# Kernel optimization log

Measured on AMD Instinct MI355X. Metric: run time of the kernel, lower is better.

The kernel has to match this reference:

```python
import jax, jax.numpy as jnp
import numpy as np

V, D, H, L, T_BLOCK = 32000, 1024, 16, 4, 1024
HD = D // H
FF = 4 * D
EPS = 1e-5


def layer_norm(x, w, b):
    mu = jnp.mean(x, axis=-1, keepdims=True)
    var = jnp.mean(jnp.square(x - mu), axis=-1, keepdims=True)
    return (x - mu) * jax.lax.rsqrt(var + EPS) * w + b


def setup_inputs() -> dict:
    key = jax.random.key(0)
    ks = iter(jax.random.split(key, 32))
    s = 0.02
    inp = {
        "idx": jax.random.randint(next(ks), (4, 1024), 0, V, dtype=jnp.int32),
        "tok_emb": jax.random.normal(next(ks), (V, D), jnp.float32) * s,
        "pos_emb": jax.random.normal(next(ks), (T_BLOCK, D), jnp.float32) * s,
        "ln1_w": jnp.ones((L, D), jnp.float32),
        "ln1_b": jnp.zeros((L, D), jnp.float32),
        "wq": jax.random.normal(next(ks), (L, D, D), jnp.float32) * s,
        "wk": jax.random.normal(next(ks), (L, D, D), jnp.float32) * s,
        "wv": jax.random.normal(next(ks), (L, D, D), jnp.float32) * s,
        "wproj": jax.random.normal(next(ks), (L, D, D), jnp.float32) * s,
        "bproj": jnp.zeros((L, D), jnp.float32),
        "ln2_w": jnp.ones((L, D), jnp.float32),
        "ln2_b": jnp.zeros((L, D), jnp.float32),
        "w1": jax.random.normal(next(ks), (L, D, FF), jnp.float32) * s,
        "b1": jnp.zeros((L, FF), jnp.float32),
        "w2": jax.random.normal(next(ks), (L, FF, D), jnp.float32) * s,
        "b2": jnp.zeros((L, D), jnp.float32),
        "lnf_w": jnp.ones((D,), jnp.float32),
        "lnf_b": jnp.zeros((D,), jnp.float32),
        "wout": jax.random.normal(next(ks), (D, V), jnp.float32) * s,
        "bout": jnp.zeros((V,), jnp.float32),
    }
    return inp


def reference(idx, tok_emb, pos_emb, ln1_w, ln1_b, wq, wk, wv, wproj, bproj,
              ln2_w, ln2_b, w1, b1, w2, b2, lnf_w, lnf_b, wout, bout):
    B, T = idx.shape
    x = tok_emb[idx] + pos_emb[:T]  # (B,T,D)
    causal = jnp.tril(jnp.ones((T, T), bool))
    scale = 1.0 / jnp.sqrt(jnp.asarray(HD, x.dtype))
    for l in range(L):
        h = layer_norm(x, ln1_w[l], ln1_b[l])
        q = (h @ wq[l]).reshape(B, T, H, HD)
        k = (h @ wk[l]).reshape(B, T, H, HD)
        v = (h @ wv[l]).reshape(B, T, H, HD)
        scores = jnp.einsum('bqhd,bkhd->bhqk', q, k) * scale
        scores = jnp.where(causal, scores, -jnp.inf)
        weights = jax.nn.softmax(scores, axis=-1)
        attn = jnp.einsum('bhqk,bkhd->bqhd', weights, v).reshape(B, T, D)
        x = x + attn @ wproj[l] + bproj[l]
        h2 = layer_norm(x, ln2_w[l], ln2_b[l])
        x = x + jax.nn.relu(h2 @ w1[l] + b1[l]) @ w2[l] + b2[l]
    x = layer_norm(x, lnf_w, lnf_b)
    logits = x @ wout + bout  # (B,T,V)
    return logits
```

## Files before the change

kernel.cpp:

```cpp
#include <hip/hip_runtime.h>
#include <hip/hip_bf16.h>

#define V_  32000
#define D_  1024
#define H_  16
#define L_  4
#define T_  1024
#define B_  4
#define HD_ 64
#define FF_ 4096
#define M_  4096
#define QP_ 3072

typedef unsigned short u16;
typedef float  f32x4   __attribute__((ext_vector_type(4)));
typedef float  f32x16  __attribute__((ext_vector_type(16)));
typedef __bf16 bf16x8  __attribute__((ext_vector_type(8)));
typedef u16    us8     __attribute__((ext_vector_type(8)));

typedef __attribute__((address_space(1))) void gvoid;
typedef __attribute__((address_space(3))) void lvoid;

__device__ __forceinline__ void glds16(const void* g, void* l) {
  __builtin_amdgcn_global_load_lds((gvoid*)g, (lvoid*)l, 16, 0, 0);
}
__device__ __forceinline__ u16 f2bf(float f) {
  __hip_bfloat16 h = __float2bfloat16(f);
  return reinterpret_cast<u16&>(h);
}

#define BAR() __builtin_amdgcn_s_barrier()
#define VMC(n) asm volatile("s_waitcnt vmcnt(" #n ")" ::: "memory")
#define LGKMC(n) do { asm volatile("s_waitcnt lgkmcnt(" #n ")" ::: "memory"); \
                      __builtin_amdgcn_sched_barrier(0); } while (0)

__global__ __launch_bounds__(256) void embed_kernel(
    const int* __restrict__ idx, const float* __restrict__ tok,
    const float* __restrict__ pos, float* __restrict__ x)
{
  int bt = blockIdx.x;
  int t  = bt & (T_ - 1);
  int id = idx[bt];
  float4 a = ((const float4*)(tok + (size_t)id * D_))[threadIdx.x];
  float4 p = ((const float4*)(pos + (size_t)t  * D_))[threadIdx.x];
  a.x += p.x; a.y += p.y; a.z += p.z; a.w += p.w;
  ((float4*)(x + (size_t)bt * D_))[threadIdx.x] = a;
}

__global__ __launch_bounds__(256) void ln_kernel(
    const float* __restrict__ x, const float* __restrict__ w,
    const float* __restrict__ b, u16* __restrict__ out)
{
  int row = blockIdx.x;
  float4 v = ((const float4*)(x + (size_t)row * D_))[threadIdx.x];
  float s  = v.x + v.y + v.z + v.w;
  float s2 = v.x * v.x + v.y * v.y + v.z * v.z + v.w * v.w;
#pragma unroll
  for (int m = 1; m < 64; m <<= 1) { s += __shfl_xor(s, m); s2 += __shfl_xor(s2, m); }
  __shared__ float ssum[4], ssum2[4];
  int wv = threadIdx.x >> 6;
  if ((threadIdx.x & 63) == 0) { ssum[wv] = s; ssum2[wv] = s2; }
  __syncthreads();
  s  = ssum[0]  + ssum[1]  + ssum[2]  + ssum[3];
  s2 = ssum2[0] + ssum2[1] + ssum2[2] + ssum2[3];
  float mu  = s * (1.f / D_);
  float var = s2 * (1.f / D_) - mu * mu;
  float rs  = rsqrtf(var + 1e-5f);
  float4 wv4 = ((const float4*)w)[threadIdx.x];
  float4 bv4 = ((const float4*)b)[threadIdx.x];
  u16* o = out + (size_t)row * D_ + threadIdx.x * 4;
  o[0] = f2bf((v.x - mu) * rs * wv4.x + bv4.x);
  o[1] = f2bf((v.y - mu) * rs * wv4.y + bv4.y);
  o[2] = f2bf((v.z - mu) * rs * wv4.z + bv4.z);
  o[3] = f2bf((v.w - mu) * rs * wv4.w + bv4.w);
}

__global__ __launch_bounds__(256) void transpose_convert(
    const float* __restrict__ in, u16* __restrict__ out, int R, int C,
    size_t inStride, size_t outStride)
{
  __shared__ float tile[32][33];
  in  += (size_t)blockIdx.z * inStride;
  out += (size_t)blockIdx.z * outStride;
  int c  = blockIdx.x * 32 + threadIdx.x;
  int r0 = blockIdx.y * 32;
#pragma unroll
  for (int j = 0; j < 4; j++)
    tile[threadIdx.y + 8 * j][threadIdx.x] =
        in[(size_t)(r0 + threadIdx.y + 8 * j) * C + c];
  __syncthreads();
  int rr = r0 + threadIdx.x;
  int cb = blockIdx.x * 32;
#pragma unroll
  for (int j = 0; j < 4; j++)
    out[(size_t)(cb + threadIdx.y + 8 * j) * R + rr] =
        f2bf(tile[threadIdx.x][threadIdx.y + 8 * j]);
}

__global__ __launch_bounds__(256) void vtrans_kernel(
    const u16* __restrict__ qkv, u16* __restrict__ vtb)
{
  __shared__ u16 tile[64][72];
  int tt = blockIdx.x, bh = blockIdx.y;
  int b = bh >> 4, h = bh & 15;
  const u16* src = qkv + ((size_t)(b * T_ + tt * 64)) * QP_ + 2 * D_ + h * HD_;
#pragma unroll
  for (int it = 0; it < 2; it++) {
    int u = it * 256 + threadIdx.x;
    int r = u >> 3, c = (u & 7) << 3;
    *(us8*)&tile[r][c] = *(const us8*)&src[(size_t)r * QP_ + c];
  }
  __syncthreads();
#pragma unroll
  for (int it = 0; it < 2; it++) {
    int u = it * 256 + threadIdx.x;
    int d = u >> 3, t8 = (u & 7) << 3;
    us8 v;
#pragma unroll
    for (int j = 0; j < 8; j++) v[j] = tile[t8 + j][d];
    *(us8*)&vtb[((size_t)bh * HD_ + d) * T_ + tt * 64 + t8] = v;
  }
}

template<int EPI>
__global__ __launch_bounds__(256) void gemm_bt(
    const u16* __restrict__ A, const u16* __restrict__ Bt,
    const float* __restrict__ bias, const float* __restrict__ resid,
    void* __restrict__ Cout, int M, int N, int K)
{
  __shared__ u16 As[128 * 32];
  __shared__ u16 Bs[128 * 32];
  const int tid = threadIdx.x;
  const int m0 = blockIdx.x * 128;
  const int n0 = blockIdx.y * 128;
  const int w = tid >> 6, lane = tid & 63, lg = lane >> 4, lr = lane & 15;
  const int wr = w >> 1, wc = w & 1;
  f32x4 acc[4][4] = {};
  const int srow = tid >> 2;
  const int scol = (tid & 3) << 3;
  const u16* ap = A  + (size_t)(m0 + srow) * K + scol;
  const u16* bp = Bt + (size_t)(n0 + srow) * K + scol;
  u16* alds  = &As[tid * 8];
  u16* alds2 = &As[2048 + tid * 8];
  u16* blds  = &Bs[tid * 8];
  u16* blds2 = &Bs[2048 + tid * 8];
  for (int k0 = 0; k0 < K; k0 += 32) {
    __syncthreads();
    glds16(ap + k0,                  alds);
    glds16(ap + (size_t)64 * K + k0, alds2);
    glds16(bp + k0,                  blds);
    glds16(bp + (size_t)64 * K + k0, blds2);
    __syncthreads();
    bf16x8 af[4], bfr[4];
#pragma unroll
    for (int i = 0; i < 4; i++)
      af[i] = *(const bf16x8*)&As[(wr * 64 + i * 16 + lr) * 32 + lg * 8];
#pragma unroll
    for (int j = 0; j < 4; j++)
      bfr[j] = *(const bf16x8*)&Bs[(wc * 64 + j * 16 + lr) * 32 + lg * 8];
#pragma unroll
    for (int i = 0; i < 4; i++)
#pragma unroll
      for (int j = 0; j < 4; j++)
        acc[i][j] = __builtin_amdgcn_mfma_f32_16x16x32_bf16(af[i], bfr[j], acc[i][j], 0, 0, 0);
  }
#pragma unroll
  for (int i = 0; i < 4; i++) {
#pragma unroll
    for (int j = 0; j < 4; j++) {
      int col = n0 + wc * 64 + j * 16 + lr;
      float bv = bias ? bias[col] : 0.f;
#pragma unroll
      for (int r = 0; r < 4; r++) {
        int row = m0 + wr * 64 + i * 16 + lg * 4 + r;
        float val = acc[i][j][r] + bv;
        size_t o = (size_t)row * N + col;
        if (EPI == 0)      ((u16*)Cout)[o]   = f2bf(val);
        else if (EPI == 1) ((u16*)Cout)[o]   = f2bf(val > 0.f ? val : 0.f);
        else if (EPI == 2) ((float*)Cout)[o] = resid[o] + val;
        else               ((float*)Cout)[o] = val;
      }
    }
  }
}

#define CLUSTER(AF, BV, MS) do { \
  __builtin_amdgcn_s_setprio(1); \
  _Pragma("unroll") for (int mq_ = 0; mq_ < 2; ++mq_) \
  _Pragma("unroll") for (int nq_ = 0; nq_ < 2; ++nq_) \
  _Pragma("unroll") for (int kq_ = 0; kq_ < 2; ++kq_) \
    acc[(MS)+mq_][nq_] = __builtin_amdgcn_mfma_f32_32x32x16_bf16( \
        AF[mq_][kq_], BV[nq_][kq_], acc[(MS)+mq_][nq_], 0, 0, 0); \
  __builtin_amdgcn_s_setprio(0); \
} while (0)

template<int EPI>
__global__ __launch_bounds__(512, 2) void gemm256(
    const u16* __restrict__ A, const u16* __restrict__ Bt,
    const float* __restrict__ bias, void* __restrict__ Cout, int N, int K)
{
  extern __shared__ char smem[];
  const int tid = threadIdx.x;
  const int nwg = gridDim.x;
  const int orig = blockIdx.x;
  const int qq = nwg >> 3, rr = nwg & 7, xcd = orig & 7, lid = orig >> 3;
  const int swz = (xcd < rr ? xcd * (qq + 1) : rr * (qq + 1) + (xcd - rr) * qq) + lid;
  const int m0 = (swz & 15) << 8;
  const int n0 = (swz >> 4) << 8;
  const int NT = K >> 6;

  const int wid = tid >> 6, lane = tid & 63;
  const int wr = wid >> 2, wc = wid & 3;
  const int l31 = lane & 31, lh = lane >> 5;
  const int gsw = (lane & 7) ^ ((lane >> 3) & 3);
  const int srow = tid >> 3, sslot = tid & 7;
  const int sg = (srow & 7) ^ ((srow >> 3) & 3);
  const int scol = ((sslot ^ sg) << 3);
  const u16* Ag = A  + (size_t)(m0 + srow) * K + scol;
  const u16* Bg = Bt + (size_t)(n0 + srow) * K + scol;
  char* ldst = smem + tid * 16;

  auto stA = [&](int bb, int kt, int h) {
    const u16* g = Ag + (size_t)(h << 7) * K + (kt << 6);
    char* l = ldst + bb * 65536 + h * 16384;
    glds16(g, l);
    glds16(g + ((size_t)K << 6), l + 8192);
  };
  auto stB = [&](int bb, int kt, int h) {
    const u16* g = Bg + (size_t)(h << 7) * K + (kt << 6);
    char* l = ldst + bb * 65536 + 32768 + h * 16384;
    glds16(g, l);
    glds16(g + ((size_t)K << 6), l + 8192);
  };
  auto ldA = [&](int bb, int mf, int ks) {
    return *(const bf16x8*)(smem + bb * 65536 +
        ((wr * 128 + mf * 32 + l31) << 7) + (((ks * 2 + lh) ^ gsw) << 4));
  };
  auto ldB = [&](int bb, int nf, int ks) {
    return *(const bf16x8*)(smem + bb * 65536 + 32768 +
        ((wc * 64 + nf * 32 + l31) << 7) + (((ks * 2 + lh) ^ gsw) << 4));
  };

  f32x16 acc[4][2] = {};
  bf16x8 afA[2][2], afB[2][2], bfvA[2][2], bfvB[2][2];

  stA(0, 0, 0); stA(0, 0, 1); stB(0, 0, 0); stB(0, 0, 1);
  VMC(0); BAR();

  for (int t = 0; t < NT; ++t) {
    const int bb = t & 1;
    if (t + 1 < NT) {
      stA(bb ^ 1, t + 1, 0); stA(bb ^ 1, t + 1, 1);
      stB(bb ^ 1, t + 1, 0); stB(bb ^ 1, t + 1, 1);
    }
#pragma unroll
    for (int i = 0; i < 2; i++) {
      afA[i][0]  = ldA(bb, i, 0);     afA[i][1]  = ldA(bb, i, 1);
      bfvA[i][0] = ldB(bb, i, 0);     bfvA[i][1] = ldB(bb, i, 1);
    }
#pragma unroll
    for (int i = 0; i < 2; i++) { afB[i][0] = ldA(bb, 2 + i, 0); afB[i][1] = ldA(bb, 2 + i, 1); }
    LGKMC(4);
    CLUSTER(afA, bfvA, 0);
#pragma unroll
    for (int i = 0; i < 2; i++) { bfvB[i][0] = ldB(bb, i, 2); bfvB[i][1] = ldB(bb, i, 3); }
#pragma unroll
    for (int i = 0; i < 2; i++) { afA[i][0] = ldA(bb, i, 2); afA[i][1] = ldA(bb, i, 3); }
    LGKMC(8);
    CLUSTER(afB, bfvA, 2);
#pragma unroll
    for (int i = 0; i < 2; i++) { afB[i][0] = ldA(bb, 2 + i, 2); afB[i][1] = ldA(bb, 2 + i, 3); }
    LGKMC(4);
    CLUSTER(afA, bfvB, 0);
    LGKMC(0);
    CLUSTER(afB, bfvB, 2);
    VMC(0); BAR();
  }

#pragma unroll
  for (int nf = 0; nf < 2; ++nf) {
    const int col = n0 + wc * 64 + nf * 32 + l31;
    const float bv = bias ? bias[col] : 0.f;
#pragma unroll
    for (int mf = 0; mf < 4; ++mf) {
#pragma unroll
      for (int v = 0; v < 16; ++v) {
        const int row = m0 + wr * 128 + mf * 32 + (v & 3) + 8 * (v >> 2) + 4 * lh;
        float val = acc[mf][nf][v] + bv;
        size_t o = (size_t)row * N + col;
        if (EPI == 0)      ((u16*)Cout)[o]   = f2bf(val);
        else if (EPI == 1) ((u16*)Cout)[o]   = f2bf(val > 0.f ? val : 0.f);
        else               __builtin_nontemporal_store(val, (float*)Cout + o);
      }
    }
  }
}

__global__ __launch_bounds__(512) void attn_kernel(
    const u16* __restrict__ qkv, const u16* __restrict__ vtb,
    u16* __restrict__ o)
{
  __shared__ u16 Ks[2][64][64];
  __shared__ u16 Vs[2][64][64];
  __shared__ u16 Ps[8][16][72];
  const int qt = blockIdx.x;
  const int bh = blockIdx.y;
  const int b = bh >> 4, h = bh & 15;
  const int tid = threadIdx.x;
  const int w = tid >> 6, lane = tid & 63, lg = lane >> 4, lr = lane & 15;
  const int q0 = qt * 128;
  const size_t qbase = ((size_t)b * T_) * QP_ + h * HD_;
  const size_t obase = ((size_t)b * T_) * D_ + h * HD_;
  const u16* qb = qkv + qbase;
  const u16* kb = qkv + qbase + D_;
  const u16* vtbh = vtb + (size_t)bh * HD_ * T_;
  bf16x8 qf[2];
  const int qrow = q0 + w * 16 + lr;
#pragma unroll
  for (int ks = 0; ks < 2; ks++)
    qf[ks] = *(const bf16x8*)&qb[(size_t)qrow * QP_ + ks * 32 + lg * 8];
  f32x4 oacc[4] = {};
  float mrun[4] = {-1e30f, -1e30f, -1e30f, -1e30f};
  float lrun[4] = {0.f, 0.f, 0.f, 0.f};
  const int srow = tid >> 3, sslot = tid & 7;
  const int sg = (srow & 7) ^ ((srow >> 3) & 3);
  const int scol = (sslot ^ sg) << 3;
  u16* kdst = &Ks[0][0][0] + tid * 8;
  u16* vdst = &Vs[0][0][0] + tid * 8;
  auto stage = [&](int kt, int bb) {
    glds16(kb + (size_t)(kt * 64 + srow) * QP_ + scol, kdst + bb * 4096);
    glds16(vtbh + (size_t)srow * T_ + kt * 64 + scol, vdst + bb * 4096);
  };
  auto ldK = [&](int bb, int j, int ks) {
    int r = j * 16 + lr;
    int g = (r & 7) ^ ((r >> 3) & 3);
    return *(const bf16x8*)&Ks[bb][r][((ks * 4 + lg) ^ g) << 3];
  };
  auto ldV = [&](int bb, int jd, int ks) {
    int r = jd * 16 + lr;
    int g = (r & 7) ^ ((r >> 3) & 3);
    return *(const bf16x8*)&Vs[bb][r][((ks * 4 + lg) ^ g) << 3];
  };

  const int ktmax = 2 * qt + 1;
  stage(0, 0);
  VMC(0); BAR();
  for (int kt = 0; kt <= ktmax; kt++) {
    const int bb = kt & 1;
    if (kt < ktmax) stage(kt + 1, bb ^ 1);
    f32x4 s[4] = {};
#pragma unroll
    for (int ks = 0; ks < 2; ks++)
#pragma unroll
      for (int j = 0; j < 4; j++)
        s[j] = __builtin_amdgcn_mfma_f32_16x16x32_bf16(qf[ks], ldK(bb, j, ks), s[j], 0, 0, 0);
#pragma unroll
    for (int j = 0; j < 4; j++) {
      int key = kt * 64 + j * 16 + lr;
#pragma unroll
      for (int r = 0; r < 4; r++) {
        int qr = q0 + w * 16 + lg * 4 + r;
        s[j][r] = (key <= qr) ? s[j][r] * 0.125f : -1e30f;
      }
    }
    float al[4];
#pragma unroll
    for (int r = 0; r < 4; r++) {
      float t0 = fmaxf(fmaxf(s[0][r], s[1][r]), fmaxf(s[2][r], s[3][r]));
#pragma unroll
      for (int m = 1; m < 16; m <<= 1) t0 = fmaxf(t0, __shfl_xor(t0, m));
      float mnew = fmaxf(mrun[r], t0);
      al[r] = __expf(mrun[r] - mnew);
      mrun[r] = mnew;
    }
#pragma unroll
    for (int j = 0; j < 4; j++)
#pragma unroll
      for (int r = 0; r < 4; r++)
        s[j][r] = __expf(s[j][r] - mrun[r]);
#pragma unroll
    for (int r = 0; r < 4; r++) {
      float rs = s[0][r] + s[1][r] + s[2][r] + s[3][r];
#pragma unroll
      for (int m = 1; m < 16; m <<= 1) rs += __shfl_xor(rs, m);
      lrun[r] = lrun[r] * al[r] + rs;
#pragma unroll
      for (int jd = 0; jd < 4; jd++) oacc[jd][r] *= al[r];
    }
#pragma unroll
    for (int j = 0; j < 4; j++)
#pragma unroll
      for (int r = 0; r < 4; r++)
        Ps[w][lg * 4 + r][j * 16 + lr] = f2bf(s[j][r]);
    asm volatile("s_waitcnt lgkmcnt(0)" ::: "memory");
    __builtin_amdgcn_sched_barrier(0);
#pragma unroll
    for (int ks = 0; ks < 2; ks++) {
      bf16x8 pf = *(const bf16x8*)&Ps[w][lr][ks * 32 + lg * 8];
#pragma unroll
      for (int jd = 0; jd < 4; jd++)
        oacc[jd] = __builtin_amdgcn_mfma_f32_16x16x32_bf16(pf, ldV(bb, jd, ks), oacc[jd], 0, 0, 0);
    }
    VMC(0); BAR();
  }
#pragma unroll
  for (int jd = 0; jd < 4; jd++)
#pragma unroll
    for (int r = 0; r < 4; r++) {
      int row = q0 + w * 16 + lg * 4 + r;
      o[obase + (size_t)row * D_ + jd * 16 + lr] = f2bf(oacc[jd][r] / lrun[r]);
    }
}

extern "C" void kernel_launch(void* const* d_in, const int* in_sizes, int n_in,
                              void* d_out, int out_size, void* d_ws, size_t ws_size,
                              hipStream_t stream)
{
  const int*   idx   = (const int*)  d_in[0];
  const float* tok   = (const float*)d_in[1];
  const float* pos   = (const float*)d_in[2];
  const float* ln1w  = (const float*)d_in[3];
  const float* ln1b  = (const float*)d_in[4];
  const float* wq    = (const float*)d_in[5];
  const float* wk    = (const float*)d_in[6];
  const float* wvw   = (const float*)d_in[7];
  const float* wproj = (const float*)d_in[8];
  const float* bproj = (const float*)d_in[9];
  const float* ln2w  = (const float*)d_in[10];
  const float* ln2b  = (const float*)d_in[11];
  const float* w1    = (const float*)d_in[12];
  const float* b1    = (const float*)d_in[13];
  const float* w2    = (const float*)d_in[14];
  const float* b2    = (const float*)d_in[15];
  const float* lnfw  = (const float*)d_in[16];
  const float* lnfb  = (const float*)d_in[17];
  const float* wout  = (const float*)d_in[18];
  const float* bout  = (const float*)d_in[19];

  hipFuncSetAttribute(reinterpret_cast<const void*>(&gemm256<0>),
                      hipFuncAttributeMaxDynamicSharedMemorySize, 131072);
  hipFuncSetAttribute(reinterpret_cast<const void*>(&gemm256<1>),
                      hipFuncAttributeMaxDynamicSharedMemorySize, 131072);
  hipFuncSetAttribute(reinterpret_cast<const void*>(&gemm256<3>),
                      hipFuncAttributeMaxDynamicSharedMemorySize, 131072);

  char* ws = (char*)d_ws;
  size_t off = 0;
  auto alloc = [&](size_t bytes) {
    void* p = ws + off;
    off += (bytes + 255) & ~(size_t)255;
    return p;
  };
  u16* wqkvT  = (u16*)alloc((size_t)L_ * 3 * D_ * D_ * 2);
  u16* wprojT = (u16*)alloc((size_t)L_ * D_ * D_ * 2);
  u16* w1T    = (u16*)alloc((size_t)L_ * D_ * FF_ * 2);
  u16* w2T    = (u16*)alloc((size_t)L_ * D_ * FF_ * 2);
  u16* woutT  = (u16*)alloc((size_t)D_ * V_ * 2);
  float* x    = (float*)alloc((size_t)M_ * D_ * 4);
  u16* hbuf   = (u16*)alloc((size_t)M_ * D_ * 2);
  u16* qkvbuf = (u16*)alloc((size_t)M_ * QP_ * 2);
  u16* vtb    = (u16*)alloc((size_t)B_ * H_ * HD_ * T_ * 2);
  u16* abuf   = (u16*)alloc((size_t)M_ * D_ * 2);
  u16* f1buf  = (u16*)alloc((size_t)M_ * FF_ * 2);

  dim3 tb(32, 8);
  const size_t DD = (size_t)D_ * D_, DF = (size_t)D_ * FF_;
  transpose_convert<<<dim3(D_ / 32, D_ / 32, L_), tb, 0, stream>>>(wq,    wqkvT,          D_,  D_, DD, 3 * DD);
  transpose_convert<<<dim3(D_ / 32, D_ / 32, L_), tb, 0, stream>>>(wk,    wqkvT + DD,     D_,  D_, DD, 3 * DD);
  transpose_convert<<<dim3(D_ / 32, D_ / 32, L_), tb, 0, stream>>>(wvw,   wqkvT + 2 * DD, D_,  D_, DD, 3 * DD);
  transpose_convert<<<dim3(D_ / 32, D_ / 32, L_), tb, 0, stream>>>(wproj, wprojT,         D_,  D_, DD, DD);
  transpose_convert<<<dim3(FF_ / 32, D_ / 32, L_), tb, 0, stream>>>(w1,   w1T,            D_,  FF_, DF, DF);
  transpose_convert<<<dim3(D_ / 32, FF_ / 32, L_), tb, 0, stream>>>(w2,   w2T,            FF_, D_, DF, DF);
  transpose_convert<<<dim3(V_ / 32, D_ / 32, 1),  tb, 0, stream>>>(wout,  woutT,          D_,  V_, 0, 0);

  embed_kernel<<<M_, 256, 0, stream>>>(idx, tok, pos, x);

  dim3 gD(M_ / 128, D_ / 128);
  for (int l = 0; l < L_; l++) {
    size_t wo = (size_t)l * DD;
    size_t fo = (size_t)l * DF;
    ln_kernel<<<M_, 256, 0, stream>>>(x, ln1w + l * D_, ln1b + l * D_, hbuf);
    gemm256<0><<<dim3(16 * (QP_ / 256)), 512, 131072, stream>>>(
        hbuf, wqkvT + (size_t)l * 3 * DD, nullptr, qkvbuf, QP_, D_);
    vtrans_kernel<<<dim3(T_ / 64, B_ * H_), 256, 0, stream>>>(qkvbuf, vtb);
    attn_kernel<<<dim3(T_ / 128, B_ * H_), 512, 0, stream>>>(qkvbuf, vtb, abuf);
    gemm_bt<2><<<gD, 256, 0, stream>>>(abuf, wprojT + wo, bproj + l * D_, x, x, M_, D_, D_);
    ln_kernel<<<M_, 256, 0, stream>>>(x, ln2w + l * D_, ln2b + l * D_, hbuf);
    gemm256<1><<<dim3(16 * (FF_ / 256)), 512, 131072, stream>>>(
        hbuf, w1T + fo, b1 + l * FF_, f1buf, FF_, D_);
    gemm_bt<2><<<gD, 256, 0, stream>>>(f1buf, w2T + fo, b2 + l * D_, x, x, M_, D_, FF_);
  }
  ln_kernel<<<M_, 256, 0, stream>>>(x, lnfw, lnfb, hbuf);
  gemm256<3><<<dim3(16 * (V_ / 256)), 512, 131072, stream>>>(
      hbuf, woutT, bout, d_out, V_, D_);
}
```

Before: 1.610 ms.

## Split-K the residual projection and FFN-down GEMMs with atomic accumulation

Replaces the residual-adding 128x128 GEMM used for the attention projection and the FFN down-projection with a split-K variant. Each K-slice block atomically adds its partial into the fp32 residual stream, and only slice 0 adds the bias. This raises the block count from 256 to 512 or 1024 so the GPU's compute units are better filled for the N=1024 outputs. The cost is many more fp32 atomic writes to global memory, and the summation order becomes nondeterministic.

```diff
diff --git a/kernel.cpp b/kernel.cpp
--- a/kernel.cpp
+++ b/kernel.cpp
@@ -122,29 +122,30 @@
   }
 }
 
-template<int EPI>
-__global__ __launch_bounds__(256) void gemm_bt(
+__global__ __launch_bounds__(256) void gemm_split(
     const u16* __restrict__ A, const u16* __restrict__ Bt,
-    const float* __restrict__ bias, const float* __restrict__ resid,
-    void* __restrict__ Cout, int M, int N, int K)
+    const float* __restrict__ bias, float* __restrict__ Cout,
+    int M, int N, int K, int splits)
 {
   __shared__ u16 As[128 * 32];
   __shared__ u16 Bs[128 * 32];
   const int tid = threadIdx.x;
   const int m0 = blockIdx.x * 128;
   const int n0 = blockIdx.y * 128;
+  const int Ksub = K / splits;
+  const int kbeg = blockIdx.z * Ksub;
   const int w = tid >> 6, lane = tid & 63, lg = lane >> 4, lr = lane & 15;
   const int wr = w >> 1, wc = w & 1;
   f32x4 acc[4][4] = {};
   const int srow = tid >> 2;
   const int scol = (tid & 3) << 3;
-  const u16* ap = A  + (size_t)(m0 + srow) * K + scol;
-  const u16* bp = Bt + (size_t)(n0 + srow) * K + scol;
+  const u16* ap = A  + (size_t)(m0 + srow) * K + kbeg + scol;
+  const u16* bp = Bt + (size_t)(n0 + srow) * K + kbeg + scol;
   u16* alds  = &As[tid * 8];
   u16* alds2 = &As[2048 + tid * 8];
   u16* blds  = &Bs[tid * 8];
   u16* blds2 = &Bs[2048 + tid * 8];
-  for (int k0 = 0; k0 < K; k0 += 32) {
+  for (int k0 = 0; k0 < Ksub; k0 += 32) {
     __syncthreads();
     glds16(ap + k0,                  alds);
     glds16(ap + (size_t)64 * K + k0, alds2);
@@ -169,16 +170,11 @@
 #pragma unroll
     for (int j = 0; j < 4; j++) {
       int col = n0 + wc * 64 + j * 16 + lr;
-      float bv = bias ? bias[col] : 0.f;
+      float bv = (blockIdx.z == 0 && bias) ? bias[col] : 0.f;
 #pragma unroll
       for (int r = 0; r < 4; r++) {
         int row = m0 + wr * 64 + i * 16 + lg * 4 + r;
-        float val = acc[i][j][r] + bv;
-        size_t o = (size_t)row * N + col;
-        if (EPI == 0)      ((u16*)Cout)[o]   = f2bf(val);
-        else if (EPI == 1) ((u16*)Cout)[o]   = f2bf(val > 0.f ? val : 0.f);
-        else if (EPI == 2) ((float*)Cout)[o] = resid[o] + val;
-        else               ((float*)Cout)[o] = val;
+        atomicAdd(Cout + (size_t)row * N + col, acc[i][j][r] + bv);
       }
     }
   }
@@ -475,7 +471,6 @@
 
   embed_kernel<<<M_, 256, 0, stream>>>(idx, tok, pos, x);
 
-  dim3 gD(M_ / 128, D_ / 128);
   for (int l = 0; l < L_; l++) {
     size_t wo = (size_t)l * DD;
     size_t fo = (size_t)l * DF;
@@ -484,11 +479,13 @@
         hbuf, wqkvT + (size_t)l * 3 * DD, nullptr, qkvbuf, QP_, D_);
     vtrans_kernel<<<dim3(T_ / 64, B_ * H_), 256, 0, stream>>>(qkvbuf, vtb);
     attn_kernel<<<dim3(T_ / 128, B_ * H_), 512, 0, stream>>>(qkvbuf, vtb, abuf);
-    gemm_bt<2><<<gD, 256, 0, stream>>>(abuf, wprojT + wo, bproj + l * D_, x, x, M_, D_, D_);
+    gemm_split<<<dim3(M_ / 128, D_ / 128, 2), 256, 0, stream>>>(
+        abuf, wprojT + wo, bproj + l * D_, x, M_, D_, D_, 2);
     ln_kernel<<<M_, 256, 0, stream>>>(x, ln2w + l * D_, ln2b + l * D_, hbuf);
     gemm256<1><<<dim3(16 * (FF_ / 256)), 512, 131072, stream>>>(
         hbuf, w1T + fo, b1 + l * FF_, f1buf, FF_, D_);
-    gemm_bt<2><<<gD, 256, 0, stream>>>(f1buf, w2T + fo, b2 + l * D_, x, x, M_, D_, FF_);
+    gemm_split<<<dim3(M_ / 128, D_ / 128, 4), 256, 0, stream>>>(
+        f1buf, w2T + fo, b2 + l * D_, x, M_, D_, FF_, 4);
   }
   ln_kernel<<<M_, 256, 0, stream>>>(x, lnfw, lnfb, hbuf);
   gemm256<3><<<dim3(16 * (V_ / 256)), 512, 131072, stream>>>(
```

Result: no change. 1.622 ms (+0.8%).

## Split-K the FFN down-projection and use 128-tile GEMM for QKV and FFN-up

Applied to the files above, without the earlier changes.

The FFN down-projection (K=4096) is split four ways along K into fp32 partial buffers, and a separate kernel sums the partials with the bias and the residual. This raises the grid from 256 to 1024 blocks to fill the GPU better. The QKV and FFN-up GEMMs move from the 256-tile pipelined gemm256 kernel to the simpler 128-tile gemm_bt, trading per-block efficiency for more blocks. The split-K path adds 64MB of partial writes and reads, and the new kernel is simple, with no double buffering.

```diff
diff --git a/kernel.cpp b/kernel.cpp
--- a/kernel.cpp
+++ b/kernel.cpp
@@ -184,6 +184,80 @@
   }
 }
 
+__global__ __launch_bounds__(256) void gemm_part(
+    const u16* __restrict__ A, const u16* __restrict__ Bt,
+    float* __restrict__ Pout, int M, int N, int K, int Ksub)
+{
+  __shared__ u16 As[128 * 32];
+  __shared__ u16 Bs[128 * 32];
+  const int tid = threadIdx.x;
+  const int m0 = blockIdx.x * 128;
+  const int n0 = blockIdx.y * 128;
+  const int kbeg = blockIdx.z * Ksub;
+  const int w = tid >> 6, lane = tid & 63, lg = lane >> 4, lr = lane & 15;
+  const int wr = w >> 1, wc = w & 1;
+  f32x4 acc[4][4] = {};
+  const int srow = tid >> 2;
+  const int scol = (tid & 3) << 3;
+  const u16* ap = A  + (size_t)(m0 + srow) * K + kbeg + scol;
+  const u16* bp = Bt + (size_t)(n0 + srow) * K + kbeg + scol;
+  u16* alds  = &As[tid * 8];
+  u16* alds2 = &As[2048 + tid * 8];
+  u16* blds  = &Bs[tid * 8];
+  u16* blds2 = &Bs[2048 + tid * 8];
+  for (int k0 = 0; k0 < Ksub; k0 += 32) {
+    __syncthreads();
+    glds16(ap + k0,                  alds);
+    glds16(ap + (size_t)64 * K + k0, alds2);
+    glds16(bp + k0,                  blds);
+    glds16(bp + (size_t)64 * K + k0, blds2);
+    __syncthreads();
+    bf16x8 af[4], bfr[4];
+#pragma unroll
+    for (int i = 0; i < 4; i++)
+      af[i] = *(const bf16x8*)&As[(wr * 64 + i * 16 + lr) * 32 + lg * 8];
+#pragma unroll
+    for (int j = 0; j < 4; j++)
+      bfr[j] = *(const bf16x8*)&Bs[(wc * 64 + j * 16 + lr) * 32 + lg * 8];
+#pragma unroll
+    for (int i = 0; i < 4; i++)
+#pragma unroll
+      for (int j = 0; j < 4; j++)
+        acc[i][j] = __builtin_amdgcn_mfma_f32_16x16x32_bf16(af[i], bfr[j], acc[i][j], 0, 0, 0);
+  }
+  float* pz = Pout + (size_t)blockIdx.z * M * N;
+#pragma unroll
+  for (int i = 0; i < 4; i++)
+#pragma unroll
+    for (int j = 0; j < 4; j++) {
+      int col = n0 + wc * 64 + j * 16 + lr;
+#pragma unroll
+      for (int r = 0; r < 4; r++) {
+        int row = m0 + wr * 64 + i * 16 + lg * 4 + r;
+        pz[(size_t)row * N + col] = acc[i][j][r];
+      }
+    }
+}
+
+__global__ __launch_bounds__(256) void reduce4_kernel(
+    const float* __restrict__ p, const float* __restrict__ bias,
+    float* __restrict__ x)
+{
+  const size_t S = (size_t)M_ * D_;
+  size_t i = ((size_t)blockIdx.x * 256 + threadIdx.x) * 4;
+  float4 v  = *(const float4*)(x + i);
+  float4 b  = *(const float4*)(bias + (i & (D_ - 1)));
+  float4 a0 = *(const float4*)(p + i);
+  float4 a1 = *(const float4*)(p + S + i);
+  float4 a2 = *(const float4*)(p + 2 * S + i);
+  float4 a3 = *(const float4*)(p + 3 * S + i);
+  v.x += a0.x + a1.x + a2.x + a3.x + b.x;
+  v.y += a0.y + a1.y + a2.y + a3.y + b.y;
+  v.z += a0.z + a1.z + a2.z + a3.z + b.z;
+  v.w += a0.w + a1.w + a2.w + a3.w + b.w;
+  *(float4*)(x + i) = v;
+}
+
 #define CLUSTER(AF, BV, MS) do { \
   __builtin_amdgcn_s_setprio(1); \
   _Pragma("unroll") for (int mq_ = 0; mq_ < 2; ++mq_) \
@@ -437,10 +511,6 @@
   const float* wout  = (const float*)d_in[18];
   const float* bout  = (const float*)d_in[19];
 
-  hipFuncSetAttribute(reinterpret_cast<const void*>(&gemm256<0>),
-                      hipFuncAttributeMaxDynamicSharedMemorySize, 131072);
-  hipFuncSetAttribute(reinterpret_cast<const void*>(&gemm256<1>),
-                      hipFuncAttributeMaxDynamicSharedMemorySize, 131072);
   hipFuncSetAttribute(reinterpret_cast<const void*>(&gemm256<3>),
                       hipFuncAttributeMaxDynamicSharedMemorySize, 131072);
 
@@ -462,6 +532,7 @@
   u16* vtb    = (u16*)alloc((size_t)B_ * H_ * HD_ * T_ * 2);
   u16* abuf   = (u16*)alloc((size_t)M_ * D_ * 2);
   u16* f1buf  = (u16*)alloc((size_t)M_ * FF_ * 2);
+  float* part = (float*)alloc((size_t)4 * M_ * D_ * 4);
 
   dim3 tb(32, 8);
   const size_t DD = (size_t)D_ * D_, DF = (size_t)D_ * FF_;
@@ -475,20 +546,22 @@
 
   embed_kernel<<<M_, 256, 0, stream>>>(idx, tok, pos, x);
 
-  dim3 gD(M_ / 128, D_ / 128);
   for (int l = 0; l < L_; l++) {
     size_t wo = (size_t)l * DD;
     size_t fo = (size_t)l * DF;
     ln_kernel<<<M_, 256, 0, stream>>>(x, ln1w + l * D_, ln1b + l * D_, hbuf);
-    gemm256<0><<<dim3(16 * (QP_ / 256)), 512, 131072, stream>>>(
-        hbuf, wqkvT + (size_t)l * 3 * DD, nullptr, qkvbuf, QP_, D_);
+    gemm_bt<0><<<dim3(M_ / 128, QP_ / 128), 256, 0, stream>>>(
+        hbuf, wqkvT + (size_t)l * 3 * DD, nullptr, nullptr, qkvbuf, M_, QP_, D_);
     vtrans_kernel<<<dim3(T_ / 64, B_ * H_), 256, 0, stream>>>(qkvbuf, vtb);
     attn_kernel<<<dim3(T_ / 128, B_ * H_), 512, 0, stream>>>(qkvbuf, vtb, abuf);
-    gemm_bt<2><<<gD, 256, 0, stream>>>(abuf, wprojT + wo, bproj + l * D_, x, x, M_, D_, D_);
+    gemm_bt<2><<<dim3(M_ / 128, D_ / 128), 256, 0, stream>>>(
+        abuf, wprojT + wo, bproj + l * D_, x, x, M_, D_, D_);
     ln_kernel<<<M_, 256, 0, stream>>>(x, ln2w + l * D_, ln2b + l * D_, hbuf);
-    gemm256<1><<<dim3(16 * (FF_ / 256)), 512, 131072, stream>>>(
-        hbuf, w1T + fo, b1 + l * FF_, f1buf, FF_, D_);
-    gemm_bt<2><<<gD, 256, 0, stream>>>(f1buf, w2T + fo, b2 + l * D_, x, x, M_, D_, FF_);
+    gemm_bt<1><<<dim3(M_ / 128, FF_ / 128), 256, 0, stream>>>(
+        hbuf, w1T + fo, b1 + l * FF_, nullptr, f1buf, M_, FF_, D_);
+    gemm_part<<<dim3(M_ / 128, D_ / 128, 4), 256, 0, stream>>>(
+        f1buf, w2T + fo, part, M_, D_, FF_, FF_ / 4);
+    reduce4_kernel<<<dim3(M_ * D_ / 1024), 256, 0, stream>>>(part, b2 + l * D_, x);
   }
   ln_kernel<<<M_, 256, 0, stream>>>(x, lnfw, lnfb, hbuf);
   gemm256<3><<<dim3(16 * (V_ / 256)), 512, 131072, stream>>>(
```

After: 1.612 ms. Within noise of the previous version (+0.1%).
